# Performance work log

Measured on AMD Instinct MI355X. Metric: run time of the kernel, lower is better.

## Reference

```python
import jax, jax.numpy as jnp
import numpy as np

NL, B, L, D, V = 8, 8, 2048, 768, 50288
HALT_ID = 50277
EPS = 1e-5


def setup_inputs() -> dict:
    key = jax.random.key(0)
    ks = jax.random.split(key, 6)
    x_steps = jax.random.normal(ks[0], (NL, B, L, D), jnp.float32)
    residual_steps = jax.random.normal(ks[1], (NL, B, L, D), jnp.float32)
    norm_weight = jnp.ones((D,), jnp.float32)
    lm_head_weight = jax.random.normal(ks[2], (V, D), jnp.float32) * 0.02
    ans_starts = jax.random.randint(ks[3], (B,), 1, L)            # valid answer positions
    chain_lens = jax.random.randint(ks[4], (B,), 1, NL + 1)       # ragged chain lengths
    chain_targets = jax.random.randint(ks[5], (B, NL), 0, V)
    # last target of each chain is <HALT> (as in training data)
    chain_targets = chain_targets.at[jnp.arange(B), chain_lens - 1].set(HALT_ID)
    return {
        "x_steps": x_steps,
        "residual_steps": residual_steps,
        "norm_weight": norm_weight,
        "lm_head_weight": lm_head_weight,
        "ans_starts": ans_starts,
        "chain_targets": chain_targets,
        "chain_lens": chain_lens,
    }


def _forward(x_steps, residual_steps, norm_weight, lm_head_weight,
             ans_starts, chain_targets, chain_lens):
    n_loops, Bn, Ln, Dn = x_steps.shape
    Vn = lm_head_weight.shape[0]
    b_idx = jnp.arange(Bn)

    # gather the single answer position per batch (logits_step[b, as_-1, :])
    pos = jnp.clip(ans_starts - 1, 0, Ln - 1)                     # [B]
    xg = x_steps[:, b_idx, pos]                                   # [NL,B,D]
    rg = residual_steps[:, b_idx, pos]                            # [NL,B,D]

    # norm_f(x, residual, prenorm=False) == RMSNorm(x + residual)
    h = xg + rg
    h = h * jax.lax.rsqrt(jnp.mean(h * h, axis=-1, keepdims=True) + EPS) * norm_weight

    # lm_head on the gathered positions only (same math as full logits + gather)
    logits = jnp.einsum("lbd,vd->lbv", h, lm_head_weight)         # [NL,B,V]

    # target id: btgt[min(loop_i, len(btgt)-1)]
    loop_i = jnp.arange(n_loops)[:, None]                         # [NL,1]
    tidx = jnp.minimum(loop_i, chain_lens[None, :] - 1)           # [NL,B]
    tgt = chain_targets[b_idx[None, :], tidx]                     # [NL,B]

    valid = (ans_starts[None, :] >= 1) & (ans_starts[None, :] < Ln) & (tgt < Vn)
    vf = valid.astype(jnp.float32)

    # full-vocab cross entropy per (loop, batch)
    logZ = jax.scipy.special.logsumexp(logits, axis=-1)           # [NL,B]
    tgt_logit = jnp.take_along_axis(logits, tgt[..., None], axis=-1)[..., 0]
    ce = logZ - tgt_logit                                         # [NL,B]

    pred = jnp.argmax(logits, axis=-1)                            # [NL,B]
    correct = (pred == tgt).astype(jnp.float32)

    cnt = vf.sum(axis=1)                                          # valid per loop
    has = cnt > 0
    hasf = has.astype(jnp.float32)
    denom = jnp.maximum(cnt, 1.0)
    loop_loss = jnp.where(has, (ce * vf).sum(axis=1) / denom, 0.0)
    loop_acc = jnp.where(has, (correct * vf).sum(axis=1) / denom, 0.0)

    n_has = hasf.sum()
    avg_loss = (loop_loss * hasf).sum() / jnp.maximum(n_has, 1.0)
    avg_acc = (loop_acc * hasf).sum() / jnp.maximum(n_has, 1.0)

    # answer_acc = mean of step_accs[:-1] (drop last valid loop) if >1 valid loop
    last_valid = n_loops - 1 - jnp.argmax(has[::-1])
    drop_last = hasf * (jnp.arange(n_loops) != last_valid).astype(jnp.float32)
    ans_mask = jnp.where(n_has > 1, drop_last, hasf)
    answer_acc = jnp.where(ans_mask.sum() > 0,
                           (loop_acc * ans_mask).sum() / jnp.maximum(ans_mask.sum(), 1.0),
                           avg_acc)

    hm = vf * (tgt == HALT_ID).astype(jnp.float32)
    halt_acc = jnp.where(hm.sum() > 0,
                         (correct * hm).sum() / jnp.maximum(hm.sum(), 1.0),
                         0.0)
    return avg_loss, avg_acc, answer_acc, halt_acc


def reference(x_steps, residual_steps, norm_weight, lm_head_weight,
              ans_starts, chain_targets, chain_lens):
    return _forward(x_steps, residual_steps, norm_weight, lm_head_weight,
                    ans_starts, chain_targets, chain_lens)
```

## Files before the change

### kernel.cpp

```cpp
#include <hip/hip_runtime.h>
#include <hip/hip_bf16.h>
#include <math.h>

#define NLOOP 8
#define BB 8
#define LLEN 2048
#define DD 768
#define VV 50288
#define HALT 50277
#define EPSF 1e-5f

#define BN 64
#define BKK 32
#define KSTEPS (DD / BKK)
#define NBLK ((VV + BN - 1) / BN)

typedef short bf16x8 __attribute__((ext_vector_type(8)));
typedef float f32x4 __attribute__((ext_vector_type(4)));

#define LGKM_BARRIER() asm volatile("s_waitcnt lgkmcnt(0)\n\ts_barrier" ::: "memory")

__device__ __forceinline__ unsigned short f32_to_bf16(float f) {
    unsigned u = __builtin_bit_cast(unsigned, f);
    unsigned r = (u + 0x7FFFu + ((u >> 16) & 1u)) >> 16;
    return (unsigned short)r;
}

__global__ __launch_bounds__(256) void k_prep(
    const float* __restrict__ x, const float* __restrict__ res,
    const float* __restrict__ nw, const float* __restrict__ W,
    const int* __restrict__ ans_starts, const int* __restrict__ chain_targets,
    const int* __restrict__ chain_lens,
    unsigned short* __restrict__ hbf, float* __restrict__ tgt_logit,
    unsigned int* __restrict__ counter)
{
    if (blockIdx.x == 0 && threadIdx.x == 0) *counter = 0u;

    int lb = blockIdx.x, l = lb >> 3, b = lb & 7;
    int tid = threadIdx.x, lane = tid & 63, wave = tid >> 6;
    int as = ans_starts[b];
    int pos = as - 1;
    pos = pos < 0 ? 0 : (pos > LLEN - 1 ? LLEN - 1 : pos);
    size_t base = ((size_t)lb * LLEN + (size_t)pos) * DD;

    float hv[3];
    float ss = 0.f;
#pragma unroll
    for (int i = 0; i < 3; ++i) {
        int d = tid + i * 256;
        float v = x[base + d] + res[base + d];
        hv[i] = v;
        ss += v * v;
    }
#pragma unroll
    for (int off = 32; off; off >>= 1) ss += __shfl_down(ss, off);
    __shared__ float red[4];
    __shared__ float bc;
    if (lane == 0) red[wave] = ss;
    __syncthreads();
    if (tid == 0) bc = red[0] + red[1] + red[2] + red[3];
    __syncthreads();
    float rs = rsqrtf(bc / (float)DD + EPSF);

    int cl = chain_lens[b];
    int tix = l < cl - 1 ? l : cl - 1;
    int tgt = chain_targets[b * NLOOP + tix];
    bool tok = (tgt >= 0) && (tgt < VV);

    float dp = 0.f;
#pragma unroll
    for (int i = 0; i < 3; ++i) {
        int d = tid + i * 256;
        float h = hv[i] * rs * nw[d];
        hbf[(size_t)lb * DD + d] = f32_to_bf16(h);
        if (tok) dp += h * W[(size_t)tgt * DD + d];
    }
#pragma unroll
    for (int off = 32; off; off >>= 1) dp += __shfl_down(dp, off);
    __syncthreads();
    if (lane == 0) red[wave] = dp;
    __syncthreads();
    if (tid == 0) tgt_logit[lb] = red[0] + red[1] + red[2] + red[3];
}

__global__ __launch_bounds__(256) void k_logits(
    const float* __restrict__ W, const unsigned short* __restrict__ hbf,
    float* __restrict__ pmax, float* __restrict__ psum, int* __restrict__ parg)
{
    __shared__ unsigned short Bs[2][64 * 56];

    int blk = blockIdx.x;
    int v0 = blk * BN;
    int tid = threadIdx.x;
    int wave = tid >> 6, lane = tid & 63, q = lane >> 4, c = lane & 15;

    const unsigned short* Ap = hbf + (size_t)(16 * wave + c) * DD + q * 8;
    bf16x8 A[KSTEPS];
#pragma unroll
    for (int ks = 0; ks < KSTEPS; ++ks)
        A[ks] = *(const bf16x8*)(Ap + ks * BKK);

    int r1 = tid >> 3, koff = (tid & 7) * 4;
    int vB0 = v0 + r1, vB1 = v0 + r1 + 32;
    const float* gB0 = W + (size_t)(vB0 < VV ? vB0 : 0) * DD + koff;
    const float* gB1 = W + (size_t)(vB1 < VV ? vB1 : 0) * DD + koff;

    f32x4 acc[4];
#pragma unroll
    for (int n = 0; n < 4; ++n) acc[n] = (f32x4){0.f, 0.f, 0.f, 0.f};

    auto stage_write = [&](int bufi, const float4& ra, const float4& rb) {
        ushort4 w0, w1;
        w0.x = f32_to_bf16(ra.x); w0.y = f32_to_bf16(ra.y);
        w0.z = f32_to_bf16(ra.z); w0.w = f32_to_bf16(ra.w);
        w1.x = f32_to_bf16(rb.x); w1.y = f32_to_bf16(rb.y);
        w1.z = f32_to_bf16(rb.z); w1.w = f32_to_bf16(rb.w);
        *(ushort4*)&Bs[bufi][r1 * 56 + koff] = w0;
        *(ushort4*)&Bs[bufi][(r1 + 32) * 56 + koff] = w1;
    };
    auto mfma_step = [&](int bufi, int ks) {
        bf16x8 f0 = *(const bf16x8*)&Bs[bufi][(c +  0) * 56 + q * 8];
        bf16x8 f1 = *(const bf16x8*)&Bs[bufi][(c + 16) * 56 + q * 8];
        bf16x8 f2 = *(const bf16x8*)&Bs[bufi][(c + 32) * 56 + q * 8];
        bf16x8 f3 = *(const bf16x8*)&Bs[bufi][(c + 48) * 56 + q * 8];
        acc[0] = __builtin_amdgcn_mfma_f32_16x16x32_bf16(A[ks], f0, acc[0], 0, 0, 0);
        acc[1] = __builtin_amdgcn_mfma_f32_16x16x32_bf16(A[ks], f1, acc[1], 0, 0, 0);
        acc[2] = __builtin_amdgcn_mfma_f32_16x16x32_bf16(A[ks], f2, acc[2], 0, 0, 0);
        acc[3] = __builtin_amdgcn_mfma_f32_16x16x32_bf16(A[ks], f3, acc[3], 0, 0, 0);
    };

    float4 pa[4], pb[4];
#pragma unroll
    for (int i = 0; i < 4; ++i) {
        pa[i] = *(const float4*)(gB0 + i * BKK);
        pb[i] = *(const float4*)(gB1 + i * BKK);
    }

#pragma unroll
    for (int ks = 0; ks < KSTEPS; ++ks) {
        const int slot = ks & 3;
        const int bufi = ks & 1;
        stage_write(bufi, pa[slot], pb[slot]);
        LGKM_BARRIER();
        if (ks + 4 < KSTEPS) {
            pa[slot] = *(const float4*)(gB0 + (ks + 4) * BKK);
            pb[slot] = *(const float4*)(gB1 + (ks + 4) * BKK);
        }
        mfma_step(bufi, ks);
    }

    const float NEGINF = -__builtin_inff();
#pragma unroll
    for (int r = 0; r < 4; ++r) {
        float val = NEGINF; int idx = 0x7fffffff;
#pragma unroll
        for (int n = 0; n < 4; ++n) {
            int colg = v0 + 16 * n + c;
            float v = (colg < VV) ? acc[n][r] : NEGINF;
            if (v > val || (v == val && colg < idx)) { val = v; idx = colg; }
        }
#pragma unroll
        for (int off = 1; off < 16; off <<= 1) {
            float ov = __shfl_xor(val, off);
            int oi = __shfl_xor(idx, off);
            if (ov > val || (ov == val && oi < idx)) { val = ov; idx = oi; }
        }
        float M = val;
        float e = 0.f;
#pragma unroll
        for (int n = 0; n < 4; ++n) {
            int colg = v0 + 16 * n + c;
            e += (colg < VV) ? __expf(acc[n][r] - M) : 0.f;
        }
#pragma unroll
        for (int off = 1; off < 16; off <<= 1) e += __shfl_xor(e, off);
        if (c == 0) {
            int row = 16 * wave + 4 * q + r;
            pmax[(size_t)row * NBLK + blk] = M;
            psum[(size_t)row * NBLK + blk] = e;
            parg[(size_t)row * NBLK + blk] = idx;
        }
    }
}

__global__ __launch_bounds__(256) void k_combine(
    const float* __restrict__ pmax, const float* __restrict__ psum,
    const int* __restrict__ parg, const float* __restrict__ tgt_logit,
    const int* __restrict__ ans_starts, const int* __restrict__ chain_targets,
    const int* __restrict__ chain_lens,
    float* __restrict__ logZ, int* __restrict__ pred,
    unsigned int* __restrict__ counter, float* __restrict__ out)
{
    int r = blockIdx.x;
    int tid = threadIdx.x;
    int wave = tid >> 6, lane = tid & 63;
    const float NEGINF = -__builtin_inff();

    const float* pm = pmax + (size_t)r * NBLK;
    const float* ps = psum + (size_t)r * NBLK;
    const int*   pa = parg + (size_t)r * NBLK;

    float M = NEGINF; int A_ = 0x7fffffff;
    for (int i = tid; i < NBLK; i += 256) {
        float m = pm[i];
        int a = pa[i];
        if (m > M || (m == M && a < A_)) { M = m; A_ = a; }
    }
#pragma unroll
    for (int off = 1; off < 64; off <<= 1) {
        float ov = __shfl_xor(M, off);
        int oa = __shfl_xor(A_, off);
        if (ov > M || (ov == M && oa < A_)) { M = ov; A_ = oa; }
    }
    __shared__ float sm[4]; __shared__ int sa[4]; __shared__ float ssum[4];
    __shared__ int lastflag;
    if (lane == 0) { sm[wave] = M; sa[wave] = A_; }
    __syncthreads();
    if (tid == 0) {
#pragma unroll
        for (int w = 1; w < 4; ++w)
            if (sm[w] > sm[0] || (sm[w] == sm[0] && sa[w] < sa[0])) { sm[0] = sm[w]; sa[0] = sa[w]; }
    }
    __syncthreads();
    float Mg = sm[0];

    float S = 0.f;
    for (int i = tid; i < NBLK; i += 256)
        S += ps[i] * __expf(pm[i] - Mg);
#pragma unroll
    for (int off = 1; off < 64; off <<= 1) S += __shfl_xor(S, off);
    if (lane == 0) ssum[wave] = S;
    __syncthreads();
    if (tid == 0) {
        float lz = Mg + logf(ssum[0] + ssum[1] + ssum[2] + ssum[3]);
        __hip_atomic_store(&logZ[r], lz, __ATOMIC_RELAXED, __HIP_MEMORY_SCOPE_AGENT);
        __hip_atomic_store(&pred[r], sa[0], __ATOMIC_RELAXED, __HIP_MEMORY_SCOPE_AGENT);
        __threadfence();
        unsigned int old = atomicAdd(counter, 1u);
        lastflag = (old == 63u) ? 1 : 0;
    }
    __syncthreads();
    if (lastflag == 0) return;

    __threadfence();
    __shared__ float lzs[64]; __shared__ int prs[64];
    if (tid < 64) {
        lzs[tid] = __hip_atomic_load(&logZ[tid], __ATOMIC_RELAXED, __HIP_MEMORY_SCOPE_AGENT);
        prs[tid] = __hip_atomic_load(&pred[tid], __ATOMIC_RELAXED, __HIP_MEMORY_SCOPE_AGENT);
    }
    __syncthreads();
    if (tid == 0) {
        float loop_loss[NLOOP], loop_acc[NLOOP], hasf[NLOOP];
        float n_has = 0.f, hms = 0.f, hcs = 0.f;
        for (int l = 0; l < NLOOP; ++l) {
            float cnt = 0.f, se = 0.f, sc = 0.f;
            for (int b = 0; b < BB; ++b) {
                int cl = chain_lens[b];
                int ti = l < cl - 1 ? l : cl - 1;
                int tgt = chain_targets[b * NLOOP + ti];
                int as = ans_starts[b];
                bool valid = (as >= 1) && (as < LLEN) && (tgt < VV);
                int idx = l * BB + b;
                float ce = lzs[idx] - tgt_logit[idx];
                float corr = (prs[idx] == tgt) ? 1.f : 0.f;
                if (valid) {
                    cnt += 1.f; se += ce; sc += corr;
                    if (tgt == HALT) { hms += 1.f; hcs += corr; }
                }
            }
            bool has = cnt > 0.f;
            hasf[l] = has ? 1.f : 0.f;
            n_has += hasf[l];
            float denom = cnt > 1.f ? cnt : 1.f;
            loop_loss[l] = has ? se / denom : 0.f;
            loop_acc[l]  = has ? sc / denom : 0.f;
        }
        float nn = n_has > 1.f ? n_has : 1.f;
        float avg_loss = 0.f, avg_acc = 0.f;
        for (int l = 0; l < NLOOP; ++l) {
            avg_loss += loop_loss[l] * hasf[l];
            avg_acc  += loop_acc[l]  * hasf[l];
        }
        avg_loss /= nn; avg_acc /= nn;
        int last_valid = NLOOP - 1;
        for (int l = NLOOP - 1; l >= 0; --l) if (hasf[l] > 0.f) { last_valid = l; break; }
        float ams = 0.f, aacc = 0.f;
        for (int l = 0; l < NLOOP; ++l) {
            float mask = (n_has > 1.f) ? (hasf[l] * ((l != last_valid) ? 1.f : 0.f)) : hasf[l];
            ams += mask; aacc += loop_acc[l] * mask;
        }
        float answer_acc = (ams > 0.f) ? (aacc / (ams > 1.f ? ams : 1.f)) : avg_acc;
        float halt_acc = (hms > 0.f) ? (hcs / (hms > 1.f ? hms : 1.f)) : 0.f;
        out[0] = avg_loss; out[1] = avg_acc; out[2] = answer_acc; out[3] = halt_acc;
    }
}

extern "C" void kernel_launch(void* const* d_in, const int* in_sizes, int n_in,
                              void* d_out, int out_size, void* d_ws, size_t ws_size,
                              hipStream_t stream) {
    const float* x   = (const float*)d_in[0];
    const float* res = (const float*)d_in[1];
    const float* nw  = (const float*)d_in[2];
    const float* W   = (const float*)d_in[3];
    const int* ans   = (const int*)d_in[4];
    const int* ct    = (const int*)d_in[5];
    const int* cl    = (const int*)d_in[6];
    float* out = (float*)d_out;

    char* ws = (char*)d_ws;
    unsigned short* hbf = (unsigned short*)ws;
    float* tgtl = (float*)(ws + 98304);
    size_t off = 98560;
    float* pmax = (float*)(ws + off);  off += (size_t)64 * NBLK * 4;
    float* psum = (float*)(ws + off);  off += (size_t)64 * NBLK * 4;
    int*   parg = (int*)  (ws + off);  off += (size_t)64 * NBLK * 4;
    float* logZ = (float*)(ws + off);  off += 256;
    int*   pred = (int*)  (ws + off);  off += 256;
    unsigned int* counter = (unsigned int*)(ws + off); off += 256;

    k_prep<<<64, 256, 0, stream>>>(x, res, nw, W, ans, ct, cl, hbf, tgtl, counter);
    k_logits<<<NBLK, 256, 0, stream>>>(W, hbf, pmax, psum, parg);
    k_combine<<<64, 256, 0, stream>>>(pmax, psum, parg, tgtl, ans, ct, cl,
                                      logZ, pred, counter, out);
}
```

Baseline: 57.81 us.

## Stream lm_head fp32 tiles into LDS via direct global-to-LDS DMA with 4-buffer pipeline

Replaces the register-staged load, convert-to-bf16 and LDS store of the weight tile with global_load_lds direct transfers of raw fp32 into a 4-deep swizzled LDS ring, three steps ahead, synchronised with vmcnt waits and barriers. The bf16 conversion moves to after the LDS read, just before each MFMA. The aim is to cut VGPR staging and conversion on the load path and to keep more memory traffic in flight. The cost is twice the LDS footprint and read bandwidth per tile and conversion work on the MFMA critical path. The XOR swizzle is there to avoid bank conflicts.

```diff
diff --git a/kernel.cpp b/kernel.cpp
--- a/kernel.cpp
+++ b/kernel.cpp
@@ -14,11 +14,11 @@
 #define BKK 32
 #define KSTEPS (DD / BKK)
 #define NBLK ((VV + BN - 1) / BN)
+#define DAHEAD 3
+#define NBUF 4
 
 typedef short bf16x8 __attribute__((ext_vector_type(8)));
 typedef float f32x4 __attribute__((ext_vector_type(4)));
-
-#define LGKM_BARRIER() asm volatile("s_waitcnt lgkmcnt(0)\n\ts_barrier" ::: "memory")
 
 __device__ __forceinline__ unsigned short f32_to_bf16(float f) {
     unsigned u = __builtin_bit_cast(unsigned, f);
@@ -87,7 +87,7 @@
     const float* __restrict__ W, const unsigned short* __restrict__ hbf,
     float* __restrict__ pmax, float* __restrict__ psum, int* __restrict__ parg)
 {
-    __shared__ unsigned short Bs[2][64 * 56];
+    __shared__ float Bs[NBUF][64 * 32];
 
     int blk = blockIdx.x;
     int v0 = blk * BN;
@@ -100,53 +100,55 @@
     for (int ks = 0; ks < KSTEPS; ++ks)
         A[ks] = *(const bf16x8*)(Ap + ks * BKK);
 
-    int r1 = tid >> 3, koff = (tid & 7) * 4;
-    int vB0 = v0 + r1, vB1 = v0 + r1 + 32;
-    const float* gB0 = W + (size_t)(vB0 < VV ? vB0 : 0) * DD + koff;
-    const float* gB1 = W + (size_t)(vB1 < VV ? vB1 : 0) * DD + koff;
+    int rl0 = wave * 16 + (lane >> 3);
+    int rl1 = rl0 + 8;
+    int g0 = v0 + rl0; if (g0 >= VV) g0 = 0;
+    int g1 = v0 + rl1; if (g1 >= VV) g1 = 0;
+    int sw0 = (lane & 7) ^ (rl0 & 6);
+    int sw1 = (lane & 7) ^ (rl1 & 6);
+    const float* p0 = W + (size_t)g0 * DD + sw0 * 4;
+    const float* p1 = W + (size_t)g1 * DD + sw1 * 4;
+
+    auto dma = [&](int ks, int buf) {
+        __builtin_amdgcn_global_load_lds(
+            (const __attribute__((address_space(1))) unsigned int*)(p0 + ks * BKK),
+            (__attribute__((address_space(3))) unsigned int*)(&Bs[buf][wave * 512]), 16, 0, 0);
+        __builtin_amdgcn_global_load_lds(
+            (const __attribute__((address_space(1))) unsigned int*)(p1 + ks * BKK),
+            (__attribute__((address_space(3))) unsigned int*)(&Bs[buf][wave * 512 + 256]), 16, 0, 0);
+    };
 
     f32x4 acc[4];
 #pragma unroll
     for (int n = 0; n < 4; ++n) acc[n] = (f32x4){0.f, 0.f, 0.f, 0.f};
 
-    auto stage_write = [&](int bufi, const float4& ra, const float4& rb) {
-        ushort4 w0, w1;
-        w0.x = f32_to_bf16(ra.x); w0.y = f32_to_bf16(ra.y);
-        w0.z = f32_to_bf16(ra.z); w0.w = f32_to_bf16(ra.w);
-        w1.x = f32_to_bf16(rb.x); w1.y = f32_to_bf16(rb.y);
-        w1.z = f32_to_bf16(rb.z); w1.w = f32_to_bf16(rb.w);
-        *(ushort4*)&Bs[bufi][r1 * 56 + koff] = w0;
-        *(ushort4*)&Bs[bufi][(r1 + 32) * 56 + koff] = w1;
+    const int slot = ((2 * q) ^ (c & 6)) * 4;
+
+    auto mfma_step = [&](int buf, int ks) {
+#pragma unroll
+        for (int n = 0; n < 4; ++n) {
+            const float* bp = &Bs[buf][(c + 16 * n) * 32 + slot];
+            f32x4 lo = *(const f32x4*)bp;
+            f32x4 hi = *(const f32x4*)(bp + 4);
+            union { bf16x8 v; __hip_bfloat162 h[4]; } u;
+            u.h[0] = __float22bfloat162_rn(make_float2(lo[0], lo[1]));
+            u.h[1] = __float22bfloat162_rn(make_float2(lo[2], lo[3]));
+            u.h[2] = __float22bfloat162_rn(make_float2(hi[0], hi[1]));
+            u.h[3] = __float22bfloat162_rn(make_float2(hi[2], hi[3]));
+            acc[n] = __builtin_amdgcn_mfma_f32_16x16x32_bf16(A[ks], u.v, acc[n], 0, 0, 0);
+        }
     };
-    auto mfma_step = [&](int bufi, int ks) {
-        bf16x8 f0 = *(const bf16x8*)&Bs[bufi][(c +  0) * 56 + q * 8];
-        bf16x8 f1 = *(const bf16x8*)&Bs[bufi][(c + 16) * 56 + q * 8];
-        bf16x8 f2 = *(const bf16x8*)&Bs[bufi][(c + 32) * 56 + q * 8];
-        bf16x8 f3 = *(const bf16x8*)&Bs[bufi][(c + 48) * 56 + q * 8];
-        acc[0] = __builtin_amdgcn_mfma_f32_16x16x32_bf16(A[ks], f0, acc[0], 0, 0, 0);
-        acc[1] = __builtin_amdgcn_mfma_f32_16x16x32_bf16(A[ks], f1, acc[1], 0, 0, 0);
-        acc[2] = __builtin_amdgcn_mfma_f32_16x16x32_bf16(A[ks], f2, acc[2], 0, 0, 0);
-        acc[3] = __builtin_amdgcn_mfma_f32_16x16x32_bf16(A[ks], f3, acc[3], 0, 0, 0);
-    };
-
-    float4 pa[4], pb[4];
-#pragma unroll
-    for (int i = 0; i < 4; ++i) {
-        pa[i] = *(const float4*)(gB0 + i * BKK);
-        pb[i] = *(const float4*)(gB1 + i * BKK);
-    }
+
+    dma(0, 0); dma(1, 1); dma(2, 2);
 
 #pragma unroll
     for (int ks = 0; ks < KSTEPS; ++ks) {
-        const int slot = ks & 3;
-        const int bufi = ks & 1;
-        stage_write(bufi, pa[slot], pb[slot]);
-        LGKM_BARRIER();
-        if (ks + 4 < KSTEPS) {
-            pa[slot] = *(const float4*)(gB0 + (ks + 4) * BKK);
-            pb[slot] = *(const float4*)(gB1 + (ks + 4) * BKK);
-        }
-        mfma_step(bufi, ks);
+        const int rem = (KSTEPS - 1 - ks) * 2;
+        if (rem >= 4)      { asm volatile("s_waitcnt vmcnt(4)\n\ts_barrier" ::: "memory"); }
+        else if (rem == 2) { asm volatile("s_waitcnt vmcnt(2)\n\ts_barrier" ::: "memory"); }
+        else               { asm volatile("s_waitcnt vmcnt(0)\n\ts_barrier" ::: "memory"); }
+        if (ks + DAHEAD < KSTEPS) dma(ks + DAHEAD, (ks + DAHEAD) & (NBUF - 1));
+        mfma_step(ks & (NBUF - 1), ks);
     }
 
     const float NEGINF = -__builtin_inff();
```

Result: slower. 59.27 us (+2.5%).
